# Optimization experiments

Measured on AMD Instinct MI355X. Metric: run time of the kernel, lower is better.

## Reference

```python
import jax, jax.numpy as jnp
import numpy as np

T = 2048          # tokens
H = 32            # query heads
HKV = 4           # kv heads
D = 128           # head dim
HID = 2048        # hidden size
EPS = 1e-6
THETA = 10000.0


def _rmsnorm(x, w):
    # x: [..., D]
    var = jnp.mean(x * x, axis=-1, keepdims=True)
    return x * jax.lax.rsqrt(var + EPS) * w


def _rope(x, positions):
    # neox-style rotary: x [T, h, D], positions [T]
    half = D // 2
    inv_freq = 1.0 / (THETA ** (jnp.arange(half, dtype=jnp.float32) * 2.0 / D))
    freqs = positions.astype(jnp.float32)[:, None] * inv_freq        # [T, D/2]
    cos = jnp.cos(freqs)[:, None, :]                                  # [T, 1, D/2]
    sin = jnp.sin(freqs)[:, None, :]
    x1, x2 = x[..., :half], x[..., half:]
    return jnp.concatenate([x1 * cos - x2 * sin, x2 * cos + x1 * sin], axis=-1)


def setup_inputs() -> dict:
    key = jax.random.key(0)
    k1, k2, k3 = jax.random.split(key, 3)
    scale_in = 1.0 / np.sqrt(HID)
    scale_o = 1.0 / np.sqrt(H * D)
    return {
        "hidden_states": jax.random.normal(k1, (T, HID), dtype=jnp.float32),
        "positions": jnp.arange(T, dtype=jnp.int32),
        "w_qkv": jax.random.normal(k2, (HID, (H + 2 * HKV) * D), dtype=jnp.float32) * scale_in,
        "w_o": jax.random.normal(k3, (H * D, HID), dtype=jnp.float32) * scale_o,
        "q_norm_w": jnp.ones((D,), dtype=jnp.float32),
        "k_norm_w": jnp.ones((D,), dtype=jnp.float32),
    }


def reference(hidden_states, positions, w_qkv, w_o, q_norm_w, k_norm_w):
    q_size, kv_size = H * D, HKV * D
    qkv = hidden_states @ w_qkv                                       # [T, (H+2*HKV)*D]
    q = qkv[:, :q_size].reshape(T, H, D)
    k = qkv[:, q_size:q_size + kv_size].reshape(T, HKV, D)
    v = qkv[:, q_size + kv_size:].reshape(T, HKV, D)

    # per-head RMSNorm on q/k, then RoPE
    q = _rope(_rmsnorm(q, q_norm_w), positions)
    k = _rope(_rmsnorm(k, k_norm_w), positions)

    # GQA: expand kv heads to query heads
    rep = H // HKV
    k = jnp.repeat(k, rep, axis=1)                                    # [T, H, D]
    v = jnp.repeat(v, rep, axis=1)

    scaling = D ** -0.5
    scores = jnp.einsum('qhd,khd->hqk', q, k) * scaling               # [H, T, T]
    causal = jnp.tril(jnp.ones((T, T), dtype=bool))
    scores = jnp.where(causal[None], scores, jnp.finfo(scores.dtype).min)
    probs = jax.nn.softmax(scores, axis=-1)
    attn = jnp.einsum('hqk,khd->qhd', probs, v).reshape(T, H * D)
    return attn @ w_o                                                 # [T, HID]
```

## Files before the change

kernel.cpp:

```cpp
#include <hip/hip_runtime.h>
#include <hip/hip_bf16.h>

typedef __attribute__((ext_vector_type(8))) __bf16 bf16x8;
typedef __attribute__((ext_vector_type(4))) __bf16 bf16x4;
typedef __attribute__((ext_vector_type(2))) __bf16 bf16x2;
typedef __attribute__((ext_vector_type(4))) float f32x4;
typedef __attribute__((ext_vector_type(16))) float f32x16;

#define T_TOK 2048
#define NH 32
#define NKV 4
#define HD 128
#define HID 2048
#define QKV_N 5120
#define QSZ 4096
#define KOFF 4096
#define VOFF 4608
#define ATT_N 4096

#define GLOAD_LDS16(g, l)                                              \
  __builtin_amdgcn_global_load_lds(                                    \
      (const __attribute__((address_space(1))) void*)(g),              \
      (__attribute__((address_space(3))) void*)(l), 16, 0, 0)

__global__ __launch_bounds__(256) void prep(const float* __restrict__ hs,
                                            __bf16* __restrict__ hsb,
                                            const float* __restrict__ wqkv,
                                            __bf16* __restrict__ wqkvT,
                                            const float* __restrict__ wo,
                                            __bf16* __restrict__ woT,
                                            const int* __restrict__ positions,
                                            float* __restrict__ tab) {
  __shared__ __attribute__((aligned(16))) __bf16 tile[64][72];
  int idx = blockIdx.x;
  if (idx < 4096) {
    int i = idx * 256 + threadIdx.x;
    float4 v = reinterpret_cast<const float4*>(hs)[i];
    bf16x4 o;
    o[0] = (__bf16)v.x; o[1] = (__bf16)v.y; o[2] = (__bf16)v.z; o[3] = (__bf16)v.w;
    reinterpret_cast<bf16x4*>(hsb)[i] = o;
    return;
  }
  idx -= 4096;
  if (idx >= 4608) {
    int j = idx - 4608;
    int t = j * 4 + (threadIdx.x >> 6);
    int d = threadIdx.x & 63;
    float freq = exp2f(-(float)d * 0.20762050593046015f);
    float fr = (float)positions[t] * freq;
    float c, s;
    sincosf(fr, &s, &c);
    tab[t * 128 + d] = c;
    tab[t * 128 + 64 + d] = s;
    return;
  }
  const float* in;
  __bf16* out;
  int R, C, bx, by;
  if (idx < 2560) { in = wqkv; out = wqkvT; R = HID; C = QKV_N; bx = idx % 80; by = idx / 80; }
  else { int j = idx - 2560; in = wo; out = woT; R = QSZ; C = HID; bx = j % 32; by = j / 32; }
  const int c0 = bx * 64;
  const int r0 = by * 64;
  const int ca = (threadIdx.x & 15) * 4;
  const int ra = (threadIdx.x >> 4) * 4;
  float4 v[4];
#pragma unroll
  for (int i = 0; i < 4; ++i)
    v[i] = *reinterpret_cast<const float4*>(&in[(size_t)(r0 + ra + i) * C + c0 + ca]);
#pragma unroll
  for (int j = 0; j < 4; ++j) {
    bf16x4 o;
#pragma unroll
    for (int i = 0; i < 4; ++i) o[i] = (__bf16)(((const float*)&v[i])[j]);
    *reinterpret_cast<bf16x4*>(&tile[ca + j][ra]) = o;
  }
  __syncthreads();
#pragma unroll
  for (int i = 0; i < 2; ++i) {
    int c = i * 32 + (threadIdx.x >> 3);
    int r8 = (threadIdx.x & 7) * 8;
    bf16x8 o = *reinterpret_cast<const bf16x8*>(&tile[c][r8]);
    *reinterpret_cast<bf16x8*>(&out[(size_t)(c0 + c) * R + r0 + r8]) = o;
  }
}

template <int MODE>
__global__ __launch_bounds__(256) void gemm_v9(const __bf16* __restrict__ A,
                                               const __bf16* __restrict__ B,
                                               void* __restrict__ Cp,
                                               int M, int N, int Ktot, int KS,
                                               int nby, int nks) {
  __shared__ __attribute__((aligned(16))) __bf16 As[3][128][32];
  __shared__ __attribute__((aligned(16))) __bf16 Bs[3][128][32];
  const int tid = threadIdx.x;
  const int lane = tid & 63;
  const int wave = tid >> 6;
  const int la = lane & 15;
  const int lb = lane >> 4;
  const int wr = (wave >> 1) * 64;
  const int wc = (wave & 1) * 64;

  const int nwg = gridDim.x;
  const int cpx = nwg >> 3;
  const int swz = ((int)blockIdx.x & 7) * cpx + ((int)blockIdx.x >> 3);
  const int ks = swz % nks;
  const int t2 = swz / nks;
  const int by = t2 % nby;
  const int bx = t2 / nby;
  const int rowA0 = by * 128;
  const int rowB0 = bx * 128;
  const int k00 = ks * KS;

  const int srow = wave * 16 + (lane >> 2);
  const int scol = (((lane & 3) * 16) ^ (((lane >> 2) & 3) << 4)) >> 1;
  const __bf16* Asrc0 = &A[(size_t)(rowA0 + srow) * Ktot + k00 + scol];
  const __bf16* Asrc1 = &A[(size_t)(rowA0 + 64 + srow) * Ktot + k00 + scol];
  const __bf16* Bsrc0 = &B[(size_t)(rowB0 + srow) * Ktot + k00 + scol];
  const __bf16* Bsrc1 = &B[(size_t)(rowB0 + 64 + srow) * Ktot + k00 + scol];

#define STAGEG(b, k0)                                            \
  do {                                                           \
    GLOAD_LDS16(Asrc0 + (k0), &As[b][wave * 16][0]);             \
    GLOAD_LDS16(Asrc1 + (k0), &As[b][64 + wave * 16][0]);        \
    GLOAD_LDS16(Bsrc0 + (k0), &Bs[b][wave * 16][0]);             \
    GLOAD_LDS16(Bsrc1 + (k0), &Bs[b][64 + wave * 16][0]);        \
  } while (0)

  f32x4 acc[4][4] = {};

  const int nt = KS >> 5;
  STAGEG(0, 0);
  STAGEG(1, 32);
  asm volatile("s_waitcnt vmcnt(4)" ::: "memory");
  __builtin_amdgcn_s_barrier();
  __builtin_amdgcn_sched_barrier(0);

  const int rdswz = (lb * 16) ^ ((la & 3) << 4);

  int cur = 0, stg = 2;
  for (int t = 0; t < nt; ++t) {
    if (t + 2 < nt) {
      STAGEG(stg, (t + 2) * 32);
    }

    const char* Ab = (const char*)&As[cur][0][0];
    const char* Bb = (const char*)&Bs[cur][0][0];
    bf16x8 af[4], bfr[4];
#pragma unroll
    for (int m = 0; m < 4; ++m)
      af[m] = *reinterpret_cast<const bf16x8*>(Ab + (wr + m * 16 + la) * 64 + rdswz);
#pragma unroll
    for (int n = 0; n < 4; ++n)
      bfr[n] = *reinterpret_cast<const bf16x8*>(Bb + (wc + n * 16 + la) * 64 + rdswz);
    __builtin_amdgcn_s_setprio(1);
#pragma unroll
    for (int m = 0; m < 4; ++m)
#pragma unroll
      for (int n = 0; n < 4; ++n)
        acc[m][n] = __builtin_amdgcn_mfma_f32_16x16x32_bf16(af[m], bfr[n], acc[m][n], 0, 0, 0);
    __builtin_amdgcn_s_setprio(0);

    const int rem = nt - 1 - t;
    if (rem >= 2) {
      asm volatile("s_waitcnt vmcnt(4)" ::: "memory");
    } else if (rem == 1) {
      asm volatile("s_waitcnt vmcnt(0)" ::: "memory");
    }
    if (rem) {
      __builtin_amdgcn_sched_barrier(0);
      __builtin_amdgcn_s_barrier();
      __builtin_amdgcn_sched_barrier(0);
    }
    cur = (cur == 2) ? 0 : cur + 1;
    stg = (stg == 2) ? 0 : stg + 1;
  }
#undef STAGEG

#pragma unroll
  for (int m = 0; m < 4; ++m) {
#pragma unroll
    for (int n = 0; n < 4; ++n) {
#pragma unroll
      for (int r = 0; r < 4; ++r) {
        int row = rowA0 + wr + m * 16 + lb * 4 + r;
        int col = rowB0 + wc + n * 16 + la;
        if (MODE == 1) {
          __bf16* pp = (__bf16*)Cp + (size_t)ks * M * N;
          pp[(size_t)row * N + col] = (__bf16)acc[m][n][r];
        } else {
          reinterpret_cast<__bf16*>(Cp)[(size_t)row * N + col] = (__bf16)acc[m][n][r];
        }
      }
    }
  }
}

__global__ __launch_bounds__(256) void reduce2_bf(const __bf16* __restrict__ pp,
                                                  float* __restrict__ out, int n8) {
  int i = blockIdx.x * 256 + threadIdx.x;
  if (i < n8) {
    bf16x8 a = reinterpret_cast<const bf16x8*>(pp)[i];
    bf16x8 b = reinterpret_cast<const bf16x8*>(pp + (size_t)HID * T_TOK)[i];
    float4 o0, o1;
    o0.x = (float)a[0] + (float)b[0];
    o0.y = (float)a[1] + (float)b[1];
    o0.z = (float)a[2] + (float)b[2];
    o0.w = (float)a[3] + (float)b[3];
    o1.x = (float)a[4] + (float)b[4];
    o1.y = (float)a[5] + (float)b[5];
    o1.z = (float)a[6] + (float)b[6];
    o1.w = (float)a[7] + (float)b[7];
    reinterpret_cast<float4*>(out)[2 * i] = o0;
    reinterpret_cast<float4*>(out)[2 * i + 1] = o1;
  }
}

__global__ __launch_bounds__(256) void postqkv(__bf16* __restrict__ qkv,
                                               __bf16* __restrict__ vt,
                                               const float* __restrict__ tab,
                                               const float* __restrict__ qw,
                                               const float* __restrict__ kw) {
  __shared__ __bf16 tile[64][72];
  int idx = blockIdx.x;
  if (idx < 18432) {
    const int t = idx & 2047;
    const int hg = idx >> 11;
    const int wave = threadIdx.x >> 6;
    const int lane = threadIdx.x & 63;
    const int head = hg * 4 + wave;
    const bool is_q = head < NH;
    const int col = is_q ? head * HD : KOFF + (head - NH) * HD;
    __bf16* row = qkv + (size_t)t * QKV_N + col;

    bf16x2 v = *reinterpret_cast<const bf16x2*>(&row[lane * 2]);
    float x0 = (float)v[0], x1 = (float)v[1];
    float ss = x0 * x0 + x1 * x1;
#pragma unroll
    for (int mm = 1; mm < 64; mm <<= 1) ss += __shfl_xor(ss, mm);
    float sc = rsqrtf(ss * (1.0f / 128.0f) + 1e-6f);
    const float* wv = is_q ? qw : kw;
    float y0 = x0 * sc * wv[lane * 2];
    float y1 = x1 * sc * wv[lane * 2 + 1];
    float o0 = __shfl_xor(y0, 32);
    float o1 = __shfl_xor(y1, 32);
    const int dbase = (lane & 31) * 2;
    float c0 = tab[t * 128 + dbase], c1 = tab[t * 128 + dbase + 1];
    float s0 = tab[t * 128 + 64 + dbase], s1 = tab[t * 128 + 64 + dbase + 1];
    float r0, r1;
    if (lane < 32) { r0 = y0 * c0 - o0 * s0; r1 = y1 * c1 - o1 * s1; }
    else           { r0 = y0 * c0 + o0 * s0; r1 = y1 * c1 + o1 * s1; }
    bf16x2 ov;
    ov[0] = (__bf16)r0;
    ov[1] = (__bf16)r1;
    *reinterpret_cast<bf16x2*>(&row[lane * 2]) = ov;
    return;
  }
  const int j = idx - 18432;
  const int t0 = (j & 31) * 64;
  const int d0 = ((j >> 5) & 1) * 64;
  const int kvh = j >> 6;
  const int tx = threadIdx.x & 63;
  const int ty = threadIdx.x >> 6;
#pragma unroll
  for (int i = 0; i < 64; i += 4)
    tile[ty + i][tx] = qkv[(size_t)(t0 + ty + i) * QKV_N + VOFF + kvh * HD + d0 + tx];
  __syncthreads();
#pragma unroll
  for (int i = 0; i < 64; i += 4)
    vt[((size_t)kvh * HD + d0 + ty + i) * T_TOK + t0 + tx] = tile[tx][ty + i];
}

__device__ __forceinline__ uint32_t pkbf(float a, float b) {
  union { __bf16 h; unsigned short u; } x, y;
  x.h = (__bf16)a;
  y.h = (__bf16)b;
  return (uint32_t)x.u | ((uint32_t)y.u << 16);
}

__global__ __launch_bounds__(256, 2) void flash_attn5(const __bf16* __restrict__ qkv,
                                                      const __bf16* __restrict__ vt,
                                                      __bf16* __restrict__ attn) {
  __shared__ __attribute__((aligned(16))) __bf16 lds[32768];

  const int tid = threadIdx.x;
  const int lane = tid & 63;
  const int wave = tid >> 6;
  const int q5 = lane & 31;
  const int hi = lane >> 5;
  const int yy = blockIdx.x;
  const int kvh = yy >> 1;
  const int h = kvh * 8 + (yy & 1) * 4 + wave;
  const __bf16* Kbase = qkv + KOFF + kvh * HD;
  const __bf16* Vbase = vt + (size_t)kvh * HD * T_TOK;

  const int qt = 63 - (int)blockIdx.y;
  const int qb = qt * 32;
  const int qrow = qb + q5;
  const int nt = (qb + 32 + 63) >> 6;

  const float qscale = 0.088388347648318447f * 1.4426950408889634f;

  bf16x8 qf[8];
  {
    const __bf16* Qp = qkv + (size_t)(qb + q5) * QKV_N + h * HD + hi * 8;
#pragma unroll
    for (int k0 = 0; k0 < 8; ++k0) {
      bf16x8 q = *reinterpret_cast<const bf16x8*>(Qp + k0 * 16);
#pragma unroll
      for (int j = 0; j < 8; ++j) q[j] = (__bf16)((float)q[j] * qscale);
      qf[k0] = q;
    }
  }

  const int kc = (lane & 15) * 16;
  const int vc = (lane & 7) * 16;

#define STAGE5(b, kv00)                                                         \
  do {                                                                          \
    __bf16* kdst = lds + (b) * 8192;                                            \
    __bf16* vdst = lds + 16384 + (b) * 8192;                                    \
    _Pragma("unroll")                                                           \
    for (int i = 0; i < 4; ++i) {                                               \
      int kr = wave * 16 + i * 4 + (lane >> 4);                                 \
      int ksc = (kc ^ ((kr & 15) << 4)) >> 1;                                   \
      GLOAD_LDS16(Kbase + (size_t)((kv00) + kr) * QKV_N + ksc,                  \
                  kdst + (wave * 16 + i * 4) * 128);                            \
      int vr = wave * 32 + i * 8 + (lane >> 3);                                 \
      int vsc = (vc ^ ((vr & 7) << 4)) >> 1;                                    \
      GLOAD_LDS16(Vbase + (size_t)vr * T_TOK + (kv00) + vsc,                    \
                  vdst + (wave * 32 + i * 8) * 64);                             \
    }                                                                           \
  } while (0)

  f32x16 acc0 = {}, acc1 = {}, acc2 = {}, acc3 = {};
  float mrow = -1e30f, lrow = 0.0f;

  STAGE5(0, 0);

  int cur = 0;
  for (int t = 0; t < nt; ++t) {
    const int kv0 = t * 64;
    __builtin_amdgcn_s_barrier();
    __builtin_amdgcn_sched_barrier(0);
    if (t + 1 < nt) {
      STAGE5(cur ^ 1, kv0 + 64);
      asm volatile("s_waitcnt vmcnt(8)" ::: "memory");
    } else {
      asm volatile("s_waitcnt vmcnt(0)" ::: "memory");
    }
    __builtin_amdgcn_s_barrier();
    __builtin_amdgcn_sched_barrier(0);

    const char* Kt = (const char*)(lds + cur * 8192);
    const char* Vt = (const char*)(lds + 16384 + cur * 8192);

    f32x16 st0 = {}, st1 = {};
    __builtin_amdgcn_s_setprio(1);
#pragma unroll
    for (int k0 = 0; k0 < 8; ++k0) {
      int cS = (k0 * 32 + hi * 16) ^ ((q5 & 15) << 4);
      bf16x8 a0 = *reinterpret_cast<const bf16x8*>(Kt + q5 * 256 + cS);
      bf16x8 a1 = *reinterpret_cast<const bf16x8*>(Kt + (32 + q5) * 256 + cS);
      st0 = __builtin_amdgcn_mfma_f32_32x32x16_bf16(a0, qf[k0], st0, 0, 0, 0);
      st1 = __builtin_amdgcn_mfma_f32_32x32x16_bf16(a1, qf[k0], st1, 0, 0, 0);
    }
    __builtin_amdgcn_s_setprio(0);

    if (!(kv0 + 63 <= qb)) {
#pragma unroll
      for (int r = 0; r < 16; ++r) {
        int kp = kv0 + (r & 3) + 8 * (r >> 2) + 4 * hi;
        if (kp > qrow) st0[r] = -1e30f;
        if (kp + 32 > qrow) st1[r] = -1e30f;
      }
    }
    float tm[16];
#pragma unroll
    for (int r = 0; r < 16; ++r) tm[r] = fmaxf(st0[r], st1[r]);
#pragma unroll
    for (int s = 8; s > 0; s >>= 1)
#pragma unroll
      for (int r = 0; r < s; ++r) tm[r] = fmaxf(tm[r], tm[r + s]);
    float mx = fmaxf(tm[0], __shfl_xor(tm[0], 32));
    if (__any(mx > mrow + 8.0f)) {
      float mnew = fmaxf(mrow, mx);
      float corr = exp2f(mrow - mnew);
      lrow *= corr;
      acc0 *= corr; acc1 *= corr; acc2 *= corr; acc3 *= corr;
      mrow = mnew;
    }
    float sv[16];
#pragma unroll
    for (int r = 0; r < 16; ++r) {
      float p0 = exp2f(st0[r] - mrow);
      float p1 = exp2f(st1[r] - mrow);
      sv[r] = p0 + p1;
      st0[r] = p0;
      st1[r] = p1;
    }
#pragma unroll
    for (int s = 8; s > 0; s >>= 1)
#pragma unroll
      for (int r = 0; r < s; ++r) sv[r] += sv[r + s];
    lrow += sv[0] + __shfl_xor(sv[0], 32);

    uint32_t W0[8], W1[8];
#pragma unroll
    for (int m = 0; m < 8; ++m) {
      W0[m] = pkbf(st0[2 * m], st0[2 * m + 1]);
      W1[m] = pkbf(st1[2 * m], st1[2 * m + 1]);
    }

    const bool hib = (hi != 0);
#pragma unroll
    for (int ks = 0; ks < 4; ++ks) {
      const int j = 4 * (ks & 1);
      uint32_t wj0, wj1, wj2, wj3;
      if (ks < 2) { wj0 = W0[j]; wj1 = W0[j + 1]; wj2 = W0[j + 2]; wj3 = W0[j + 3]; }
      else        { wj0 = W1[j]; wj1 = W1[j + 1]; wj2 = W1[j + 2]; wj3 = W1[j + 3]; }
      uint32_t keepA = hib ? wj2 : wj0;
      uint32_t keepB = hib ? wj3 : wj1;
      uint32_t sendA = hib ? wj0 : wj2;
      uint32_t sendB = hib ? wj1 : wj3;
      uint32_t recvA = (uint32_t)__shfl_xor((int)sendA, 32);
      uint32_t recvB = (uint32_t)__shfl_xor((int)sendB, 32);
      union { uint32_t u[4]; bf16x8 v; } fr;
      fr.u[0] = hib ? recvA : keepA;
      fr.u[1] = hib ? recvB : keepB;
      fr.u[2] = hib ? keepA : recvA;
      fr.u[3] = hib ? keepB : recvB;
      const int cV = (ks * 32 + hi * 16) ^ ((q5 & 7) << 4);
      __builtin_amdgcn_s_setprio(1);
      bf16x8 v0 = *reinterpret_cast<const bf16x8*>(Vt + (0 * 32 + q5) * 128 + cV);
      acc0 = __builtin_amdgcn_mfma_f32_32x32x16_bf16(v0, fr.v, acc0, 0, 0, 0);
      bf16x8 v1 = *reinterpret_cast<const bf16x8*>(Vt + (1 * 32 + q5) * 128 + cV);
      acc1 = __builtin_amdgcn_mfma_f32_32x32x16_bf16(v1, fr.v, acc1, 0, 0, 0);
      bf16x8 v2 = *reinterpret_cast<const bf16x8*>(Vt + (2 * 32 + q5) * 128 + cV);
      acc2 = __builtin_amdgcn_mfma_f32_32x32x16_bf16(v2, fr.v, acc2, 0, 0, 0);
      bf16x8 v3 = *reinterpret_cast<const bf16x8*>(Vt + (3 * 32 + q5) * 128 + cV);
      acc3 = __builtin_amdgcn_mfma_f32_32x32x16_bf16(v3, fr.v, acc3, 0, 0, 0);
      __builtin_amdgcn_s_setprio(0);
    }
    cur ^= 1;
  }

  __syncthreads();
  {
    char* ob = (char*)lds + wave * 8192;
    float inv = 1.0f / lrow;
    const int swzE = (q5 & 15) << 4;
#pragma unroll
    for (int dt = 0; dt < 4; ++dt) {
      f32x16 a = dt == 0 ? acc0 : dt == 1 ? acc1 : dt == 2 ? acc2 : acc3;
#pragma unroll
      for (int t4 = 0; t4 < 4; ++t4) {
        uint2 wv;
        wv.x = pkbf(a[4 * t4] * inv, a[4 * t4 + 1] * inv);
        wv.y = pkbf(a[4 * t4 + 2] * inv, a[4 * t4 + 3] * inv);
        int d2 = (dt * 32 + 8 * t4 + 4 * hi) * 2;
        *reinterpret_cast<uint2*>(ob + q5 * 256 + (d2 ^ swzE)) = wv;
      }
    }
#pragma unroll
    for (int rr = 0; rr < 8; ++rr) {
      int idx = rr * 64 + lane;
      int q = idx >> 4;
      int cc = (idx & 15) * 16;
      bf16x8 o = *reinterpret_cast<const bf16x8*>(ob + q * 256 + (cc ^ ((q & 15) << 4)));
      *reinterpret_cast<bf16x8*>(&attn[(size_t)(qb + q) * ATT_N + h * HD + (cc >> 1)]) = o;
    }
  }
}

extern "C" void kernel_launch(void* const* d_in, const int* in_sizes, int n_in,
                              void* d_out, int out_size, void* d_ws, size_t ws_size,
                              hipStream_t stream) {
  const float* hs   = (const float*)d_in[0];
  const int*   pos  = (const int*)d_in[1];
  const float* wqkv = (const float*)d_in[2];
  const float* wo   = (const float*)d_in[3];
  const float* qw   = (const float*)d_in[4];
  const float* kw   = (const float*)d_in[5];
  float* out = (float*)d_out;

  char* p = (char*)d_ws;
  __bf16* hsb   = (__bf16*)p; p += (size_t)T_TOK * HID * 2;
  __bf16* wqkvT = (__bf16*)p; p += (size_t)QKV_N * HID * 2;
  __bf16* woT   = (__bf16*)p; p += (size_t)HID * QSZ * 2;
  __bf16* qkvb  = (__bf16*)p; p += (size_t)T_TOK * QKV_N * 2;
  __bf16* attnb = (__bf16*)p; p += (size_t)T_TOK * QSZ * 2;
  __bf16* vtb   = (__bf16*)p; p += (size_t)NKV * HD * T_TOK * 2;
  float*  ropet = (float*)p;  p += (size_t)T_TOK * HD * 4;
  __bf16* oprt  = (__bf16*)p; p += (size_t)2 * T_TOK * HID * 2;

  prep<<<9216, 256, 0, stream>>>(hs, hsb, wqkv, wqkvT, wo, woT, pos, ropet);
  gemm_v9<0><<<(QKV_N / 128) * (T_TOK / 128), 256, 0, stream>>>(
      hsb, wqkvT, qkvb, T_TOK, QKV_N, HID, HID, T_TOK / 128, 1);
  postqkv<<<18688, 256, 0, stream>>>(qkvb, vtb, ropet, qw, kw);
  flash_attn5<<<dim3(8, 64), 256, 0, stream>>>(qkvb, vtb, attnb);
  gemm_v9<1><<<2 * (HID / 128) * (T_TOK / 128), 256, 0, stream>>>(
      attnb, woT, oprt, T_TOK, HID, QSZ, QSZ / 2, T_TOK / 128, 2);
  reduce2_bf<<<(T_TOK * HID / 8 + 255) / 256, 256, 0, stream>>>(
      oprt, out, T_TOK * HID / 8);
}
```

Measured before the change: 225.3 us.

## Split long causal attention rows across two KV halves and merge partials

The flash attention kernel now splits the KV range for the upper 32 query tiles into two halves handled by separate blocks. Those blocks write unnormalized partial outputs plus per-row max and sum, and a new merge kernel combines them. The aim is to balance the causal triangle's uneven work and raise the grid size. LDS use drops to a single K buffer with double-buffered V, moving to 3 blocks per CU, and the sync schedule changes. This adds an extra kernel launch, partial-output traffic, and a bf16 rounding step on the unnormalized partials.

```diff
diff --git a/kernel.cpp b/kernel.cpp
--- a/kernel.cpp
+++ b/kernel.cpp
@@ -277,10 +277,12 @@
   return (uint32_t)x.u | ((uint32_t)y.u << 16);
 }
 
-__global__ __launch_bounds__(256, 2) void flash_attn5(const __bf16* __restrict__ qkv,
+__global__ __launch_bounds__(256, 3) void flash_attn8(const __bf16* __restrict__ qkv,
                                                       const __bf16* __restrict__ vt,
-                                                      __bf16* __restrict__ attn) {
-  __shared__ __attribute__((aligned(16))) __bf16 lds[32768];
+                                                      __bf16* __restrict__ attn,
+                                                      __bf16* __restrict__ pO,
+                                                      float2* __restrict__ ml) {
+  __shared__ __attribute__((aligned(16))) __bf16 lds[24576];
 
   const int tid = threadIdx.x;
   const int lane = tid & 63;
@@ -293,10 +295,17 @@
   const __bf16* Kbase = qkv + KOFF + kvh * HD;
   const __bf16* Vbase = vt + (size_t)kvh * HD * T_TOK;
 
-  const int qt = 63 - (int)blockIdx.y;
+  int qt, part;
+  {
+    const int y = blockIdx.y;
+    if (y < 64) { qt = 63 - (y >> 1); part = y & 1; }
+    else        { qt = 95 - y;        part = -1;     }
+  }
   const int qb = qt * 32;
   const int qrow = qb + q5;
-  const int nt = (qb + 32 + 63) >> 6;
+  const int nt = (qb + 95) >> 6;
+  int t0 = 0, t1 = nt;
+  if (part >= 0) { const int nh = nt >> 1; if (part) t0 = nh; else t1 = nh; }
 
   const float qscale = 0.088388347648318447f * 1.4426950408889634f;
 
@@ -315,44 +324,41 @@
   const int kc = (lane & 15) * 16;
   const int vc = (lane & 7) * 16;
 
-#define STAGE5(b, kv00)                                                         \
-  do {                                                                          \
-    __bf16* kdst = lds + (b) * 8192;                                            \
-    __bf16* vdst = lds + 16384 + (b) * 8192;                                    \
-    _Pragma("unroll")                                                           \
-    for (int i = 0; i < 4; ++i) {                                               \
-      int kr = wave * 16 + i * 4 + (lane >> 4);                                 \
-      int ksc = (kc ^ ((kr & 15) << 4)) >> 1;                                   \
-      GLOAD_LDS16(Kbase + (size_t)((kv00) + kr) * QKV_N + ksc,                  \
-                  kdst + (wave * 16 + i * 4) * 128);                            \
-      int vr = wave * 32 + i * 8 + (lane >> 3);                                 \
-      int vsc = (vc ^ ((vr & 7) << 4)) >> 1;                                    \
-      GLOAD_LDS16(Vbase + (size_t)vr * T_TOK + (kv00) + vsc,                    \
-                  vdst + (wave * 32 + i * 8) * 64);                             \
-    }                                                                           \
+#define STAGEK(kv00)                                                     \
+  do {                                                                   \
+    _Pragma("unroll")                                                    \
+    for (int i = 0; i < 4; ++i) {                                        \
+      int kr = wave * 16 + i * 4 + (lane >> 4);                          \
+      int ksc = (kc ^ ((kr & 15) << 4)) >> 1;                            \
+      GLOAD_LDS16(Kbase + (size_t)((kv00) + kr) * QKV_N + ksc,           \
+                  lds + (wave * 16 + i * 4) * 128);                      \
+    }                                                                    \
+  } while (0)
+#define STAGEV(kv00, par)                                                \
+  do {                                                                   \
+    __bf16* vdst = lds + 8192 + (par) * 8192;                            \
+    _Pragma("unroll")                                                    \
+    for (int i = 0; i < 4; ++i) {                                        \
+      int vr = wave * 32 + i * 8 + (lane >> 3);                          \
+      int vsc = (vc ^ ((vr & 7) << 4)) >> 1;                             \
+      GLOAD_LDS16(Vbase + (size_t)vr * T_TOK + (kv00) + vsc,             \
+                  vdst + (wave * 32 + i * 8) * 64);                      \
+    }                                                                    \
   } while (0)
 
   f32x16 acc0 = {}, acc1 = {}, acc2 = {}, acc3 = {};
   float mrow = -1e30f, lrow = 0.0f;
 
-  STAGE5(0, 0);
-
-  int cur = 0;
-  for (int t = 0; t < nt; ++t) {
+  STAGEK(t0 * 64);
+  STAGEV(t0 * 64, t0 & 1);
+  asm volatile("s_waitcnt vmcnt(0)" ::: "memory");
+  __builtin_amdgcn_s_barrier();
+  __builtin_amdgcn_sched_barrier(0);
+
+  for (int t = t0; t < t1; ++t) {
     const int kv0 = t * 64;
-    __builtin_amdgcn_s_barrier();
-    __builtin_amdgcn_sched_barrier(0);
-    if (t + 1 < nt) {
-      STAGE5(cur ^ 1, kv0 + 64);
-      asm volatile("s_waitcnt vmcnt(8)" ::: "memory");
-    } else {
-      asm volatile("s_waitcnt vmcnt(0)" ::: "memory");
-    }
-    __builtin_amdgcn_s_barrier();
-    __builtin_amdgcn_sched_barrier(0);
-
-    const char* Kt = (const char*)(lds + cur * 8192);
-    const char* Vt = (const char*)(lds + 16384 + cur * 8192);
+    const char* Kt = (const char*)lds;
+    const char* Vt = (const char*)lds + 16384 + (t & 1) * 16384;
 
     f32x16 st0 = {}, st1 = {};
     __builtin_amdgcn_s_setprio(1);
@@ -365,6 +371,14 @@
       st1 = __builtin_amdgcn_mfma_f32_32x32x16_bf16(a1, qf[k0], st1, 0, 0, 0);
     }
     __builtin_amdgcn_s_setprio(0);
+
+    __builtin_amdgcn_sched_barrier(0);
+    __builtin_amdgcn_s_barrier();
+    __builtin_amdgcn_sched_barrier(0);
+    if (t + 1 < t1) {
+      STAGEK((t + 1) * 64);
+      STAGEV((t + 1) * 64, (t + 1) & 1);
+    }
 
     if (!(kv0 + 63 <= qb)) {
 #pragma unroll
@@ -441,35 +455,91 @@
       acc3 = __builtin_amdgcn_mfma_f32_32x32x16_bf16(v3, fr.v, acc3, 0, 0, 0);
       __builtin_amdgcn_s_setprio(0);
     }
-    cur ^= 1;
-  }
+    if (t + 1 < t1) {
+      asm volatile("s_waitcnt vmcnt(0)" ::: "memory");
+    }
+    __builtin_amdgcn_sched_barrier(0);
+    __builtin_amdgcn_s_barrier();
+    __builtin_amdgcn_sched_barrier(0);
+  }
+#undef STAGEK
+#undef STAGEV
 
   __syncthreads();
   {
     char* ob = (char*)lds + wave * 8192;
-    float inv = 1.0f / lrow;
     const int swzE = (q5 & 15) << 4;
+    const float sc = (part < 0) ? (1.0f / lrow) : 1.0f;
 #pragma unroll
     for (int dt = 0; dt < 4; ++dt) {
       f32x16 a = dt == 0 ? acc0 : dt == 1 ? acc1 : dt == 2 ? acc2 : acc3;
 #pragma unroll
       for (int t4 = 0; t4 < 4; ++t4) {
         uint2 wv;
-        wv.x = pkbf(a[4 * t4] * inv, a[4 * t4 + 1] * inv);
-        wv.y = pkbf(a[4 * t4 + 2] * inv, a[4 * t4 + 3] * inv);
+        wv.x = pkbf(a[4 * t4] * sc, a[4 * t4 + 1] * sc);
+        wv.y = pkbf(a[4 * t4 + 2] * sc, a[4 * t4 + 3] * sc);
         int d2 = (dt * 32 + 8 * t4 + 4 * hi) * 2;
         *reinterpret_cast<uint2*>(ob + q5 * 256 + (d2 ^ swzE)) = wv;
       }
     }
-#pragma unroll
-    for (int rr = 0; rr < 8; ++rr) {
-      int idx = rr * 64 + lane;
-      int q = idx >> 4;
-      int cc = (idx & 15) * 16;
-      bf16x8 o = *reinterpret_cast<const bf16x8*>(ob + q * 256 + (cc ^ ((q & 15) << 4)));
-      *reinterpret_cast<bf16x8*>(&attn[(size_t)(qb + q) * ATT_N + h * HD + (cc >> 1)]) = o;
-    }
-  }
+    if (part < 0) {
+#pragma unroll
+      for (int rr = 0; rr < 8; ++rr) {
+        int idx = rr * 64 + lane;
+        int q = idx >> 4;
+        int cc = (idx & 15) * 16;
+        bf16x8 o = *reinterpret_cast<const bf16x8*>(ob + q * 256 + (cc ^ ((q & 15) << 4)));
+        *reinterpret_cast<bf16x8*>(&attn[(size_t)(qb + q) * ATT_N + h * HD + (cc >> 1)]) = o;
+      }
+    } else {
+      const int pq = qt - 32;
+      const size_t slot = ((size_t)(part * 32 + pq) * NH + h) * 32;
+      __bf16* pb = pO + slot * 128;
+#pragma unroll
+      for (int rr = 0; rr < 8; ++rr) {
+        int idx = rr * 64 + lane;
+        int q = idx >> 4;
+        int cc = (idx & 15) * 16;
+        bf16x8 o = *reinterpret_cast<const bf16x8*>(ob + q * 256 + (cc ^ ((q & 15) << 4)));
+        *reinterpret_cast<bf16x8*>(&pb[(size_t)q * 128 + (cc >> 1)]) = o;
+      }
+      if (hi == 0) ml[slot + q5] = make_float2(mrow, lrow);
+    }
+  }
+}
+
+__global__ __launch_bounds__(256) void merge_attn(const __bf16* __restrict__ pO,
+                                                  const float2* __restrict__ ml,
+                                                  __bf16* __restrict__ attn) {
+  const int b = blockIdx.x;
+  const int pq = b >> 5;
+  const int h = b & 31;
+  const int q = threadIdx.x >> 3;
+  const int dd = (threadIdx.x & 7) * 16;
+  const size_t s0 = ((size_t)pq * NH + h) * 32 + q;
+  const size_t s1 = ((size_t)(32 + pq) * NH + h) * 32 + q;
+  float2 a0 = ml[s0];
+  float2 a1 = ml[s1];
+  float M = fmaxf(a0.x, a1.x);
+  float w0 = exp2f(a0.x - M);
+  float w1 = exp2f(a1.x - M);
+  float inv = 1.0f / (a0.y * w0 + a1.y * w1);
+  w0 *= inv;
+  w1 *= inv;
+  bf16x8 x0a = *reinterpret_cast<const bf16x8*>(&pO[s0 * 128 + dd]);
+  bf16x8 x0b = *reinterpret_cast<const bf16x8*>(&pO[s0 * 128 + dd + 8]);
+  bf16x8 x1a = *reinterpret_cast<const bf16x8*>(&pO[s1 * 128 + dd]);
+  bf16x8 x1b = *reinterpret_cast<const bf16x8*>(&pO[s1 * 128 + dd + 8]);
+  bf16x8 oa, obv;
+#pragma unroll
+  for (int j = 0; j < 8; ++j) {
+    oa[j] = (__bf16)((float)x0a[j] * w0 + (float)x1a[j] * w1);
+    obv[j] = (__bf16)((float)x0b[j] * w0 + (float)x1b[j] * w1);
+  }
+  const int row = (pq + 32) * 32 + q;
+  __bf16* dst = attn + (size_t)row * ATT_N + h * HD + dd;
+  *reinterpret_cast<bf16x8*>(dst) = oa;
+  *reinterpret_cast<bf16x8*>(dst + 8) = obv;
 }
 
 extern "C" void kernel_launch(void* const* d_in, const int* in_sizes, int n_in,
@@ -492,12 +562,15 @@
   __bf16* vtb   = (__bf16*)p; p += (size_t)NKV * HD * T_TOK * 2;
   float*  ropet = (float*)p;  p += (size_t)T_TOK * HD * 4;
   __bf16* oprt  = (__bf16*)p; p += (size_t)2 * T_TOK * HID * 2;
+  __bf16* pOb   = (__bf16*)p; p += (size_t)2 * 32 * NH * 32 * 128 * 2;
+  float2* mlb   = (float2*)p; p += (size_t)2 * 32 * NH * 32 * sizeof(float2);
 
   prep<<<9216, 256, 0, stream>>>(hs, hsb, wqkv, wqkvT, wo, woT, pos, ropet);
   gemm_v9<0><<<(QKV_N / 128) * (T_TOK / 128), 256, 0, stream>>>(
       hsb, wqkvT, qkvb, T_TOK, QKV_N, HID, HID, T_TOK / 128, 1);
   postqkv<<<18688, 256, 0, stream>>>(qkvb, vtb, ropet, qw, kw);
-  flash_attn5<<<dim3(8, 64), 256, 0, stream>>>(qkvb, vtb, attnb);
+  flash_attn8<<<dim3(8, 96), 256, 0, stream>>>(qkvb, vtb, attnb, pOb, mlb);
+  merge_attn<<<1024, 256, 0, stream>>>(pOb, mlb, attnb);
   gemm_v9<1><<<2 * (HID / 128) * (T_TOK / 128), 256, 0, stream>>>(
       attnb, woT, oprt, T_TOK, HID, QSZ, QSZ / 2, T_TOK / 128, 2);
   reduce2_bf<<<(T_TOK * HID / 8 + 255) / 256, 256, 0, stream>>>(
```

After: 230.3 us. 2.2% more time.
